# Kernel tuning notes

Measured on AMD Instinct MI355X. Metric: run time of the kernel, lower is better.

Reference implementation:

```python
import jax, jax.numpy as jnp
import numpy as np

B, L, H, E = 32, 2048, 1024, 512


def setup_inputs() -> dict:
    key = jax.random.key(0)
    ks = jax.random.split(key, 11)
    s = 0.02
    return {
        "h": jax.random.normal(ks[0], (B, H), jnp.float32),
        "x": jax.random.normal(ks[1], (B, E), jnp.float32),
        "contexts": jax.random.normal(ks[2], (B, L, H), jnp.float32),
        "W_enc": jax.random.normal(ks[3], (H, H), jnp.float32) * s,
        "b_enc": jnp.zeros((H,), jnp.float32),
        "W_dec": jax.random.normal(ks[4], (H, H), jnp.float32) * s,
        "b_dec": jnp.zeros((H,), jnp.float32),
        "W_v": jax.random.normal(ks[5], (H,), jnp.float32) * s,  # linear_v weight, out_dim=1
        "b_v": jnp.zeros((), jnp.float32),
        "W_r": jax.random.normal(ks[6], (2 * H + E, 2 * H), jnp.float32) * s,
        "b_r": jnp.zeros((2 * H,), jnp.float32),
    }


def reference(h, x, contexts, W_enc, b_enc, W_dec, b_dec, W_v, b_v, W_r, b_r):
    # additive (Bahdanau) score: v^T tanh(W_e @ ctx + W_d @ h)
    gamma_enc = jnp.einsum("blh,hk->blk", contexts, W_enc) + b_enc       # [B,L,H]
    gamma_dec = (h @ W_dec + b_dec)[:, None, :]                           # [B,1,H]
    scores = jnp.tanh(gamma_enc + gamma_dec) @ W_v + b_v                  # [B,L]
    weights = jax.nn.softmax(scores, axis=1)                              # [B,L]
    c_t = jnp.einsum("bl,blh->bh", weights, contexts)                     # [B,H]
    r_t = jnp.concatenate([c_t, h, x], axis=1) @ W_r + b_r                # [B,2H]
    # maxout: view(-1, H, 2).max(2)
    output = jnp.max(r_t.reshape(-1, H, 2), axis=2)                       # [B,H]
    return output, weights
```

## Files before the change

kernel.cpp:

```cpp
#include <hip/hip_runtime.h>
#include <hip/hip_bf16.h>

typedef unsigned short u16;
typedef __attribute__((ext_vector_type(8))) short bf16x8;
typedef __attribute__((ext_vector_type(4))) float f32x4;

#define B_   32
#define L_   2048
#define H_   1024
#define E_   512
#define KCAT 2560
#define NR   2048

__device__ __align__(256) u16   g_WencT[H_*H_];
__device__ __align__(256) float g_gdec[B_*H_];
__device__ __align__(256) float g_scores[B_*L_];
__device__ __align__(256) float g_cat[B_*KCAT];
__device__ __align__(256) float g_pct[32][B_*H_];
__device__ __align__(256) float g_part[40][B_*NR];

__device__ __forceinline__ u16 f2b(float f) {
  unsigned x = __float_as_uint(f);
  return (u16)((x + 0x7fffu + ((x >> 16) & 1u)) >> 16);
}

__device__ __forceinline__ void gll16(const void* g, void* l) {
  __builtin_amdgcn_global_load_lds(
      (const __attribute__((address_space(1))) void*)g,
      (__attribute__((address_space(3))) void*)l, 16, 0, 0);
}

__device__ __forceinline__ float tanh_fast(float x) {
  float e = __expf(2.0f * x);
  return 1.0f - 2.0f / (e + 1.0f);
}

__global__ __launch_bounds__(256) void k_transpose(const float* __restrict__ W) {
  __shared__ float t[64 * 65];
  const int n0 = blockIdx.x * 64, k0 = blockIdx.y * 64;
  const int c = threadIdx.x & 63, q = threadIdx.x >> 6;
  #pragma unroll
  for (int rr = 0; rr < 16; rr++) {
    int r = rr * 4 + q;
    t[c * 65 + r] = W[(size_t)(k0 + r) * H_ + n0 + c];
  }
  __syncthreads();
  #pragma unroll
  for (int nn = 0; nn < 16; nn++) {
    int nl = nn * 4 + q;
    g_WencT[(size_t)(n0 + nl) * H_ + k0 + c] = f2b(t[nl * 65 + c]);
  }
}

__global__ __launch_bounds__(256) void k_init(const float* __restrict__ h,
                                              const float* __restrict__ x,
                                              const float* __restrict__ b_enc,
                                              const float* __restrict__ b_dec,
                                              const float* __restrict__ b_v) {
  int id = blockIdx.x * 256 + threadIdx.x;
  if (id < 32768) { g_gdec[id] = b_dec[id & 1023] + b_enc[id & 1023]; return; }
  id -= 32768;
  if (id < 65536) { g_scores[id] = b_v[0]; return; }
  id -= 65536;
  {
    int b = id / KCAT, c = id - b * KCAT;
    float v = 0.0f;
    if (c >= 1024 && c < 2048) v = h[b * H_ + (c - 1024)];
    else if (c >= 2048)        v = x[b * E_ + (c - 2048)];
    g_cat[id] = v;
  }
}

__global__ __launch_bounds__(256) void k_gdec(const float* __restrict__ h,
                                              const float* __restrict__ Wd) {
  const int b = blockIdx.y;
  const int hc = blockIdx.x & 3, kc = blockIdx.x >> 2;
  const int col = hc * 256 + threadIdx.x;
  const float* hb = h + b * H_ + kc * 256;
  const float* wp = Wd + (size_t)(kc * 256) * H_ + col;
  float acc = 0.0f;
  #pragma unroll 4
  for (int k = 0; k < 256; k++) acc = fmaf(hb[k], wp[(size_t)k * H_], acc);
  atomicAdd(&g_gdec[b * H_ + col], acc);
}

__global__ __launch_bounds__(1024, 4) void k_scores(const float* __restrict__ ctx,
                                                    const float* __restrict__ Wv) {
  __shared__ u16 Ab[2][64 * 32];
  __shared__ u16 Bb[2][1024 * 32];
  __shared__ float ssum[64];
  const int tid = threadIdx.x;
  const int bid = blockIdx.x;
  const int b  = bid >> 5;
  const int l0 = (bid & 31) << 6;
  if (tid < 64) ssum[tid] = 0.0f;

  const int arow = tid >> 4, akp = tid & 15;
  const float* actx = ctx + ((size_t)(b * L_ + l0 + arow)) * H_ + akp * 2;
  const unsigned aidx = arow * 32 + ((akp * 2) ^ ((arow & 3) << 3));

  const unsigned bnl = tid >> 2, bslot = tid & 3;

  f32x4 acc[4][4];
  #pragma unroll
  for (int i = 0; i < 4; i++) {
    #pragma unroll
    for (int j = 0; j < 4; j++) acc[i][j] = (f32x4)0.0f;
  }

  const int lane = tid & 63;
  const int w    = tid >> 6;
  const int r16  = lane & 15;
  const int g8   = (lane >> 4) * 8;

  auto stageB = [&](int buf, int ks) {
    const unsigned k0b = ks * 64;
    #pragma unroll
    for (int q = 0; q < 4; q++) {
      unsigned nl = q * 256 + bnl;
      unsigned ga = nl * 2048 + k0b + ((bslot ^ (nl & 3)) << 4);
      gll16((const char*)g_WencT + ga, (char*)&Bb[buf][0] + q * 16384 + tid * 16);
    }
  };

  {
    float2 av = *(const float2*)actx;
    stageB(0, 0);
    *(ushort2*)&Ab[0][aidx] = make_ushort2(f2b(av.x), f2b(av.y));
  }
  __syncthreads();

  #pragma unroll 2
  for (int ks = 0; ks < 32; ks++) {
    const int cur = ks & 1;
    float2 av;
    if (ks < 31) {
      av = *(const float2*)(actx + (ks + 1) * 32);
      stageB(cur ^ 1, ks + 1);
    }
    bf16x8 af[4], bfv[4];
    #pragma unroll
    for (int mt = 0; mt < 4; mt++) {
      int row = mt * 16 + r16;
      af[mt] = *(const bf16x8*)&Ab[cur][row * 32 + (g8 ^ ((row & 3) << 3))];
    }
    #pragma unroll
    for (int nt = 0; nt < 4; nt++) {
      int col = w * 64 + nt * 16 + r16;
      bfv[nt] = *(const bf16x8*)&Bb[cur][col * 32 + (g8 ^ ((col & 3) << 3))];
    }
    #pragma unroll
    for (int mt = 0; mt < 4; mt++) {
      #pragma unroll
      for (int nt = 0; nt < 4; nt++)
        acc[mt][nt] = __builtin_amdgcn_mfma_f32_16x16x32_bf16(af[mt], bfv[nt],
                                                              acc[mt][nt], 0, 0, 0);
    }
    if (ks < 31) {
      *(ushort2*)&Ab[cur ^ 1][aidx] = make_ushort2(f2b(av.x), f2b(av.y));
    }
    __syncthreads();
  }

  float wv[4], gd[4];
  #pragma unroll
  for (int nt = 0; nt < 4; nt++) {
    int col = w * 64 + nt * 16 + r16;
    wv[nt] = Wv[col];
    gd[nt] = g_gdec[b * H_ + col];
  }
  const int rbase = (lane >> 4) * 4;
  #pragma unroll
  for (int mt = 0; mt < 4; mt++) {
    #pragma unroll
    for (int r = 0; r < 4; r++) {
      float p = 0.0f;
      #pragma unroll
      for (int nt = 0; nt < 4; nt++)
        p += tanh_fast(acc[mt][nt][r] + gd[nt]) * wv[nt];
      p += __shfl_xor(p, 1);
      p += __shfl_xor(p, 2);
      p += __shfl_xor(p, 4);
      p += __shfl_xor(p, 8);
      if (r16 == 0) atomicAdd(&ssum[mt * 16 + rbase + r], p);
    }
  }
  __syncthreads();
  if (tid < 64) atomicAdd(&g_scores[b * L_ + l0 + tid], ssum[tid]);
}

__global__ __launch_bounds__(256) void k_softmax(float* __restrict__ wout) {
  const int b = blockIdx.x, tid = threadIdx.x;
  __shared__ float red[4];
  float v[8]; float m = -1e30f;
  #pragma unroll
  for (int i = 0; i < 8; i++) {
    v[i] = g_scores[b * L_ + i * 256 + tid];
    m = fmaxf(m, v[i]);
  }
  #pragma unroll
  for (int s = 1; s < 64; s <<= 1) m = fmaxf(m, __shfl_xor(m, s));
  if ((tid & 63) == 0) red[tid >> 6] = m;
  __syncthreads();
  m = fmaxf(fmaxf(red[0], red[1]), fmaxf(red[2], red[3]));
  __syncthreads();
  float s = 0.0f;
  #pragma unroll
  for (int i = 0; i < 8; i++) { v[i] = __expf(v[i] - m); s += v[i]; }
  #pragma unroll
  for (int t = 1; t < 64; t <<= 1) s += __shfl_xor(s, t);
  if ((tid & 63) == 0) red[tid >> 6] = s;
  __syncthreads();
  const float inv = 1.0f / (red[0] + red[1] + red[2] + red[3]);
  #pragma unroll
  for (int i = 0; i < 8; i++) wout[b * L_ + i * 256 + tid] = v[i] * inv;
}

__global__ __launch_bounds__(256) void k_ct(const float* __restrict__ ctx,
                                            const float* __restrict__ wout) {
  const int lc = blockIdx.x, b = blockIdx.y, tid = threadIdx.x;
  const int l0 = lc * 64;
  __shared__ float wl[64];
  if (tid < 64) wl[tid] = wout[b * L_ + l0 + tid];
  __syncthreads();
  const float4* cp = (const float4*)(ctx + ((size_t)(b * L_ + l0)) * H_) + tid;
  float4 a = {0.f, 0.f, 0.f, 0.f};
  #pragma unroll 4
  for (int i = 0; i < 64; i++) {
    float4 vv = cp[(size_t)i * 256];
    float wv = wl[i];
    a.x = fmaf(vv.x, wv, a.x);
    a.y = fmaf(vv.y, wv, a.y);
    a.z = fmaf(vv.z, wv, a.z);
    a.w = fmaf(vv.w, wv, a.w);
  }
  *(float4*)&g_pct[lc][b * H_ + tid * 4] = a;
}

__global__ __launch_bounds__(256) void k_ctred() {
  const int id = blockIdx.x * 256 + threadIdx.x;
  float s = 0.0f;
  #pragma unroll 8
  for (int lc = 0; lc < 32; lc++) s += g_pct[lc][id];
  g_cat[(id >> 10) * KCAT + (id & 1023)] = s;
}

__global__ __launch_bounds__(256) void k_r1(const float* __restrict__ Wr) {
  const int nc = blockIdx.x, kc = blockIdx.y, tid = threadIdx.x;
  __shared__ float cl[32][64];
  #pragma unroll
  for (int i = 0; i < 8; i++) {
    int flat = i * 256 + tid;
    cl[flat >> 6][flat & 63] = g_cat[(flat >> 6) * KCAT + kc * 64 + (flat & 63)];
  }
  __syncthreads();
  float acc[32];
  #pragma unroll
  for (int b2 = 0; b2 < 32; b2++) acc[b2] = 0.0f;
  const float* wp = Wr + (size_t)(kc * 64) * NR + nc * 256 + tid;
  #pragma unroll 4
  for (int k4 = 0; k4 < 16; k4++) {
    float w0 = wp[(size_t)(k4 * 4 + 0) * NR], w1 = wp[(size_t)(k4 * 4 + 1) * NR],
          w2 = wp[(size_t)(k4 * 4 + 2) * NR], w3 = wp[(size_t)(k4 * 4 + 3) * NR];
    #pragma unroll
    for (int b2 = 0; b2 < 32; b2++) {
      const float4 c4 = *(const float4*)&cl[b2][k4 * 4];
      acc[b2] = fmaf(c4.x, w0, acc[b2]);
      acc[b2] = fmaf(c4.y, w1, acc[b2]);
      acc[b2] = fmaf(c4.z, w2, acc[b2]);
      acc[b2] = fmaf(c4.w, w3, acc[b2]);
    }
  }
  float* pp = &g_part[kc][nc * 256 + tid];
  #pragma unroll
  for (int b2 = 0; b2 < 32; b2++) pp[b2 * NR] = acc[b2];
}

__global__ __launch_bounds__(256) void k_maxout(const float* __restrict__ b_r,
                                                float* __restrict__ out) {
  const int id = blockIdx.x * 256 + threadIdx.x;
  const int j = id & 1023;
  float r0 = b_r[2 * j], r1 = b_r[2 * j + 1];
  #pragma unroll 8
  for (int kc = 0; kc < 40; kc++) {
    const float2 v = *(const float2*)&g_part[kc][2 * id];
    r0 += v.x; r1 += v.y;
  }
  out[id] = fmaxf(r0, r1);
}

extern "C" void kernel_launch(void* const* d_in, const int* in_sizes, int n_in,
                              void* d_out, int out_size, void* d_ws, size_t ws_size,
                              hipStream_t stream) {
  (void)in_sizes; (void)n_in; (void)d_ws; (void)ws_size; (void)out_size;
  const float* h     = (const float*)d_in[0];
  const float* x     = (const float*)d_in[1];
  const float* ctx   = (const float*)d_in[2];
  const float* W_enc = (const float*)d_in[3];
  const float* b_enc = (const float*)d_in[4];
  const float* W_dec = (const float*)d_in[5];
  const float* b_dec = (const float*)d_in[6];
  const float* W_v   = (const float*)d_in[7];
  const float* b_v   = (const float*)d_in[8];
  const float* W_r   = (const float*)d_in[9];
  const float* b_r   = (const float*)d_in[10];
  float* out  = (float*)d_out;
  float* wout = out + 32768;

  k_transpose<<<dim3(16, 16), 256, 0, stream>>>(W_enc);
  k_init<<<704, 256, 0, stream>>>(h, x, b_enc, b_dec, b_v);
  k_gdec<<<dim3(16, 32), 256, 0, stream>>>(h, W_dec);
  k_scores<<<1024, 1024, 0, stream>>>(ctx, W_v);
  k_softmax<<<32, 256, 0, stream>>>(wout);
  k_ct<<<dim3(32, 32), 256, 0, stream>>>(ctx, wout);
  k_ctred<<<128, 256, 0, stream>>>();
  k_r1<<<dim3(8, 40), 256, 0, stream>>>(W_r);
  k_maxout<<<128, 256, 0, stream>>>(b_r, out);
}
```

Measured before the change: 739.2 us.

## Pre-convert contexts to bf16 and retile scores GEMM to 256x256 blocks

```diff
diff --git a/kernel.cpp b/kernel.cpp
--- a/kernel.cpp
+++ b/kernel.cpp
@@ -13,6 +13,7 @@
 #define NR   2048
 
 __device__ __align__(256) u16   g_WencT[H_*H_];
+__device__ __align__(256) u16   g_ctx16[(size_t)B_*L_*H_];
 __device__ __align__(256) float g_gdec[B_*H_];
 __device__ __align__(256) float g_scores[B_*L_];
 __device__ __align__(256) float g_cat[B_*KCAT];
@@ -23,6 +24,9 @@
   unsigned x = __float_as_uint(f);
   return (u16)((x + 0x7fffu + ((x >> 16) & 1u)) >> 16);
 }
+__device__ __forceinline__ float b2f(u16 u) {
+  return __uint_as_float(((unsigned)u) << 16);
+}
 
 __device__ __forceinline__ void gll16(const void* g, void* l) {
   __builtin_amdgcn_global_load_lds(
@@ -49,6 +53,22 @@
   for (int nn = 0; nn < 16; nn++) {
     int nl = nn * 4 + q;
     g_WencT[(size_t)(n0 + nl) * H_ + k0 + c] = f2b(t[nl * 65 + c]);
+  }
+}
+
+__global__ __launch_bounds__(256) void k_cvt(const float* __restrict__ ctx) {
+  const size_t gid = (size_t)blockIdx.x * 256 + threadIdx.x;
+  #pragma unroll
+  for (int it = 0; it < 8; it++) {
+    const size_t c = gid + (size_t)it * 1048576;
+    const float4 a = *(const float4*)(ctx + c * 8);
+    const float4 b = *(const float4*)(ctx + c * 8 + 4);
+    bf16x8 o;
+    o[0] = (short)f2b(a.x); o[1] = (short)f2b(a.y);
+    o[2] = (short)f2b(a.z); o[3] = (short)f2b(a.w);
+    o[4] = (short)f2b(b.x); o[5] = (short)f2b(b.y);
+    o[6] = (short)f2b(b.z); o[7] = (short)f2b(b.w);
+    *(bf16x8*)&g_ctx16[c * 8] = o;
   }
 }
 
@@ -79,114 +99,110 @@
   const float* hb = h + b * H_ + kc * 256;
   const float* wp = Wd + (size_t)(kc * 256) * H_ + col;
   float acc = 0.0f;
-  #pragma unroll 4
+  #pragma unroll 8
   for (int k = 0; k < 256; k++) acc = fmaf(hb[k], wp[(size_t)k * H_], acc);
   atomicAdd(&g_gdec[b * H_ + col], acc);
 }
 
-__global__ __launch_bounds__(1024, 4) void k_scores(const float* __restrict__ ctx,
-                                                    const float* __restrict__ Wv) {
-  __shared__ u16 Ab[2][64 * 32];
-  __shared__ u16 Bb[2][1024 * 32];
-  __shared__ float ssum[64];
+#define BK 64
+__global__ __launch_bounds__(512, 2) void k_scores(const float* __restrict__ Wv) {
+  __shared__ u16 Ab[2][256 * BK];
+  __shared__ u16 Bb[2][256 * BK];
+  __shared__ float ssum[256];
   const int tid = threadIdx.x;
-  const int bid = blockIdx.x;
-  const int b  = bid >> 5;
-  const int l0 = (bid & 31) << 6;
-  if (tid < 64) ssum[tid] = 0.0f;
-
-  const int arow = tid >> 4, akp = tid & 15;
-  const float* actx = ctx + ((size_t)(b * L_ + l0 + arow)) * H_ + akp * 2;
-  const unsigned aidx = arow * 32 + ((akp * 2) ^ ((arow & 3) << 3));
-
-  const unsigned bnl = tid >> 2, bslot = tid & 3;
-
-  f32x4 acc[4][4];
-  #pragma unroll
-  for (int i = 0; i < 4; i++) {
+
+  const int orig = blockIdx.x;
+  const int wg = (orig & 7) * 128 + (orig >> 3);
+  const int mtile = wg >> 2;
+  const int ntile = wg & 3;
+  const int b  = mtile >> 3;
+  const int l0 = (mtile & 7) * 256;
+
+  const char* Asrc = (const char*)(g_ctx16 + ((size_t)(b * L_ + l0)) * H_);
+  const char* Bsrc = (const char*)(g_WencT + (size_t)(ntile * 256) * H_);
+
+  size_t soff[4];
+  #pragma unroll
+  for (int q = 0; q < 4; q++) {
+    const int sid = q * 512 + tid;
+    const int row = sid >> 3, slot = sid & 7;
+    soff[q] = (size_t)row * 2048 + (size_t)((slot ^ (row & 7)) << 4);
+  }
+
+  const int lane = tid & 63, wid = tid >> 6;
+  const int wm = wid >> 2, wn = wid & 3;
+  const int r16 = lane & 15, g = lane >> 4;
+  const int base_a = (wm * 128 + r16) * BK;
+  const int base_b = (wn * 64 + r16) * BK;
+
+  if (tid < 256) ssum[tid] = 0.0f;
+
+  f32x4 acc[8][4];
+  #pragma unroll
+  for (int i = 0; i < 8; i++)
     #pragma unroll
     for (int j = 0; j < 4; j++) acc[i][j] = (f32x4)0.0f;
-  }
-
-  const int lane = tid & 63;
-  const int w    = tid >> 6;
-  const int r16  = lane & 15;
-  const int g8   = (lane >> 4) * 8;
-
-  auto stageB = [&](int buf, int ks) {
-    const unsigned k0b = ks * 64;
-    #pragma unroll
-    for (int q = 0; q < 4; q++) {
-      unsigned nl = q * 256 + bnl;
-      unsigned ga = nl * 2048 + k0b + ((bslot ^ (nl & 3)) << 4);
-      gll16((const char*)g_WencT + ga, (char*)&Bb[buf][0] + q * 16384 + tid * 16);
-    }
+
+  auto stage = [&](int buf, int ks) {
+    const size_t kb = (size_t)ks * 128;
+    #pragma unroll
+    for (int q = 0; q < 4; q++)
+      gll16(Asrc + soff[q] + kb, (char*)&Ab[buf][0] + q * 8192 + tid * 16);
+    #pragma unroll
+    for (int q = 0; q < 4; q++)
+      gll16(Bsrc + soff[q] + kb, (char*)&Bb[buf][0] + q * 8192 + tid * 16);
   };
 
-  {
-    float2 av = *(const float2*)actx;
-    stageB(0, 0);
-    *(ushort2*)&Ab[0][aidx] = make_ushort2(f2b(av.x), f2b(av.y));
-  }
-  __syncthreads();
-
-  #pragma unroll 2
-  for (int ks = 0; ks < 32; ks++) {
+  stage(0, 0);
+  __syncthreads();
+
+  for (int ks = 0; ks < 16; ks++) {
     const int cur = ks & 1;
-    float2 av;
-    if (ks < 31) {
-      av = *(const float2*)(actx + (ks + 1) * 32);
-      stageB(cur ^ 1, ks + 1);
-    }
-    bf16x8 af[4], bfv[4];
-    #pragma unroll
-    for (int mt = 0; mt < 4; mt++) {
-      int row = mt * 16 + r16;
-      af[mt] = *(const bf16x8*)&Ab[cur][row * 32 + (g8 ^ ((row & 3) << 3))];
-    }
-    #pragma unroll
-    for (int nt = 0; nt < 4; nt++) {
-      int col = w * 64 + nt * 16 + r16;
-      bfv[nt] = *(const bf16x8*)&Bb[cur][col * 32 + (g8 ^ ((col & 3) << 3))];
-    }
-    #pragma unroll
-    for (int mt = 0; mt < 4; mt++) {
+    if (ks < 15) stage(cur ^ 1, ks + 1);
+    #pragma unroll
+    for (int kk = 0; kk < 2; kk++) {
+      const int po = (((kk * 4 + g) ^ (r16 & 7)) << 3);
+      bf16x8 bf0 = *(const bf16x8*)&Bb[cur][base_b + 0 * 1024 + po];
+      bf16x8 bf1 = *(const bf16x8*)&Bb[cur][base_b + 1 * 1024 + po];
+      bf16x8 bf2 = *(const bf16x8*)&Bb[cur][base_b + 2 * 1024 + po];
+      bf16x8 bf3 = *(const bf16x8*)&Bb[cur][base_b + 3 * 1024 + po];
       #pragma unroll
-      for (int nt = 0; nt < 4; nt++)
-        acc[mt][nt] = __builtin_amdgcn_mfma_f32_16x16x32_bf16(af[mt], bfv[nt],
-                                                              acc[mt][nt], 0, 0, 0);
-    }
-    if (ks < 31) {
-      *(ushort2*)&Ab[cur ^ 1][aidx] = make_ushort2(f2b(av.x), f2b(av.y));
+      for (int mt = 0; mt < 8; mt++) {
+        bf16x8 am = *(const bf16x8*)&Ab[cur][base_a + mt * 1024 + po];
+        acc[mt][0] = __builtin_amdgcn_mfma_f32_16x16x32_bf16(am, bf0, acc[mt][0], 0, 0, 0);
+        acc[mt][1] = __builtin_amdgcn_mfma_f32_16x16x32_bf16(am, bf1, acc[mt][1], 0, 0, 0);
+        acc[mt][2] = __builtin_amdgcn_mfma_f32_16x16x32_bf16(am, bf2, acc[mt][2], 0, 0, 0);
+        acc[mt][3] = __builtin_amdgcn_mfma_f32_16x16x32_bf16(am, bf3, acc[mt][3], 0, 0, 0);
+      }
     }
     __syncthreads();
   }
 
+  const int colb = ntile * 256 + wn * 64;
   float wv[4], gd[4];
   #pragma unroll
-  for (int nt = 0; nt < 4; nt++) {
-    int col = w * 64 + nt * 16 + r16;
-    wv[nt] = Wv[col];
-    gd[nt] = g_gdec[b * H_ + col];
-  }
-  const int rbase = (lane >> 4) * 4;
-  #pragma unroll
-  for (int mt = 0; mt < 4; mt++) {
+  for (int q = 0; q < 4; q++) {
+    const int col = colb + q * 16 + r16;
+    wv[q] = Wv[col];
+    gd[q] = g_gdec[b * H_ + col];
+  }
+  #pragma unroll
+  for (int mt = 0; mt < 8; mt++) {
     #pragma unroll
     for (int r = 0; r < 4; r++) {
       float p = 0.0f;
       #pragma unroll
-      for (int nt = 0; nt < 4; nt++)
-        p += tanh_fast(acc[mt][nt][r] + gd[nt]) * wv[nt];
+      for (int q = 0; q < 4; q++)
+        p += tanh_fast(acc[mt][q][r] + gd[q]) * wv[q];
       p += __shfl_xor(p, 1);
       p += __shfl_xor(p, 2);
       p += __shfl_xor(p, 4);
       p += __shfl_xor(p, 8);
-      if (r16 == 0) atomicAdd(&ssum[mt * 16 + rbase + r], p);
+      if (r16 == 0) atomicAdd(&ssum[wm * 128 + mt * 16 + g * 4 + r], p);
     }
   }
   __syncthreads();
-  if (tid < 64) atomicAdd(&g_scores[b * L_ + l0 + tid], ssum[tid]);
+  if (tid < 256) atomicAdd(&g_scores[b * L_ + l0 + tid], ssum[tid]);
 }
 
 __global__ __launch_bounds__(256) void k_softmax(float* __restrict__ wout) {
@@ -216,25 +232,24 @@
   for (int i = 0; i < 8; i++) wout[b * L_ + i * 256 + tid] = v[i] * inv;
 }
 
-__global__ __launch_bounds__(256) void k_ct(const float* __restrict__ ctx,
-                                            const float* __restrict__ wout) {
-  const int lc = blockIdx.x, b = blockIdx.y, tid = threadIdx.x;
-  const int l0 = lc * 64;
-  __shared__ float wl[64];
-  if (tid < 64) wl[tid] = wout[b * L_ + l0 + tid];
-  __syncthreads();
-  const float4* cp = (const float4*)(ctx + ((size_t)(b * L_ + l0)) * H_) + tid;
-  float4 a = {0.f, 0.f, 0.f, 0.f};
-  #pragma unroll 4
+__global__ __launch_bounds__(256) void k_ct(const float* __restrict__ wout) {
+  const int lc = blockIdx.x, b = blockIdx.y;
+  const int cg = threadIdx.x & 127, rh = threadIdx.x >> 7;
+  __shared__ float wl[128];
+  if (threadIdx.x < 128) wl[threadIdx.x] = wout[b * L_ + lc * 128 + threadIdx.x];
+  __syncthreads();
+  const u16* cp = g_ctx16 + ((size_t)(b * L_ + lc * 128 + rh * 64)) * H_ + cg * 8;
+  float a[8] = {0.f, 0.f, 0.f, 0.f, 0.f, 0.f, 0.f, 0.f};
+  #pragma unroll 8
   for (int i = 0; i < 64; i++) {
-    float4 vv = cp[(size_t)i * 256];
-    float wv = wl[i];
-    a.x = fmaf(vv.x, wv, a.x);
-    a.y = fmaf(vv.y, wv, a.y);
-    a.z = fmaf(vv.z, wv, a.z);
-    a.w = fmaf(vv.w, wv, a.w);
-  }
-  *(float4*)&g_pct[lc][b * H_ + tid * 4] = a;
+    const bf16x8 v = *(const bf16x8*)(cp + (size_t)i * H_);
+    const float w = wl[rh * 64 + i];
+    #pragma unroll
+    for (int j = 0; j < 8; j++) a[j] = fmaf(b2f((u16)v[j]), w, a[j]);
+  }
+  #pragma unroll
+  for (int j = 0; j < 8; j++)
+    g_pct[lc * 2 + rh][b * H_ + cg * 8 + j] = a[j];
 }
 
 __global__ __launch_bounds__(256) void k_ctred() {
@@ -308,11 +323,12 @@
   float* wout = out + 32768;
 
   k_transpose<<<dim3(16, 16), 256, 0, stream>>>(W_enc);
+  k_cvt<<<4096, 256, 0, stream>>>(ctx);
   k_init<<<704, 256, 0, stream>>>(h, x, b_enc, b_dec, b_v);
   k_gdec<<<dim3(16, 32), 256, 0, stream>>>(h, W_dec);
-  k_scores<<<1024, 1024, 0, stream>>>(ctx, W_v);
+  k_scores<<<1024, 512, 0, stream>>>(W_v);
   k_softmax<<<32, 256, 0, stream>>>(wout);
-  k_ct<<<dim3(32, 32), 256, 0, stream>>>(ctx, wout);
+  k_ct<<<dim3(16, 32), 256, 0, stream>>>(wout);
   k_ctred<<<128, 256, 0, stream>>>();
   k_r1<<<dim3(8, 40), 256, 0, stream>>>(W_r);
   k_maxout<<<128, 256, 0, stream>>>(b_r, out);
```

After: 669.3 us. 9.5% less time.
